# Optimization experiments

Hardware: AMD Instinct MI355X
Metric: run time of the kernel (lower is better)

The kernel has to match this reference:

```python
import jax, jax.numpy as jnp
import numpy as np

KG_E = 50000
KG_R = 500
E_DIM = 300
NE = 400000      # entity-entity adjacency nnz
NEER = 400000    # entity-entity-relation triples
ALPHA1 = 0.1
ALPHA2 = 0.3
LRELU_ALPHA = 0.2


def setup_inputs() -> dict:
    key = jax.random.key(0)
    ks = jax.random.split(key, 13)
    primal_e_0 = jax.random.normal(ks[0], (KG_E, E_DIM), jnp.float32)
    # sparse-ish relation->entity incidence matrices (dense storage as in torch code)
    r_head = (jax.random.uniform(ks[1], (KG_R, KG_E)) < 0.01).astype(jnp.float32)
    r_tail = (jax.random.uniform(ks[2], (KG_R, KG_E)) < 0.01).astype(jnp.float32)
    e_adj_index = jax.random.randint(ks[3], (2, NE), 0, KG_E)
    e_adj_data = jax.random.uniform(ks[4], (NE,), jnp.float32)
    eer_adj_index = jax.random.randint(ks[5], (2, NEER), 0, KG_E)
    eer_adj_data = jax.random.randint(ks[6], (NEER,), 0, KG_R)
    s = 0.05
    be_L = jax.random.normal(ks[7], (KG_E, 1), jnp.float32) * s
    be_R = jax.random.normal(ks[8], (KG_E, 1), jnp.float32) * s
    atten_r = jax.random.normal(ks[9], (2 * E_DIM, 1), jnp.float32) * s
    gcnW1 = jax.random.normal(ks[10], (E_DIM, E_DIM), jnp.float32) * s
    highwayWr = jax.random.normal(ks[11], (E_DIM, E_DIM), jnp.float32) * s
    highwaybr = jax.random.normal(ks[12], (E_DIM, 1), jnp.float32) * s
    return {"primal_e_0": primal_e_0, "r_head": r_head, "r_tail": r_tail,
            "e_adj_data": e_adj_data, "be_L": be_L, "be_R": be_R,
            "atten_r": atten_r, "gcnW1": gcnW1, "highwayWr": highwayWr,
            "highwaybr": highwaybr, "e_adj_index": e_adj_index,
            "eer_adj_index": eer_adj_index, "eer_adj_data": eer_adj_data}


def _spmm(idx, data, x):
    # sparse [KG_E, KG_E] (COO rows=idx[0], cols=idx[1], vals=data) @ dense x
    rows, cols = idx[0], idx[1]
    return jax.ops.segment_sum(data[:, None] * x[cols], rows, num_segments=KG_E)


def _inv_or_zero(x):
    return jnp.where(x == 0, 0.0, 1.0 / x)


def _add_r_layer(e, be_L, be_R, r_head, r_tail, rh_inv, rt_inv):
    L_r = (r_head @ (e * be_L)) * rh_inv   # [KG_R, E_DIM]
    R_r = (r_tail @ (e * be_R)) * rt_inv
    return jax.nn.relu(jnp.concatenate([L_r, R_r], axis=-1))  # [KG_R, 2*E_DIM]


def _add_e_att_layer(e, r_layer, eer_idx, eer_rel, atten_r):
    rows, cols = eer_idx[0], eer_idx[1]
    e_ij = jnp.concatenate([e[rows], e[cols]], axis=1)           # [NEER, 2*E_DIM]
    eer_embed = e_ij * r_layer[eer_rel]                           # [NEER, 2*E_DIM]
    score = (eer_embed @ atten_r)[:, 0]                           # [NEER]
    ee_atten = jnp.exp(-jax.nn.leaky_relu(score, LRELU_ALPHA))
    e_rowsum = jax.ops.segment_sum(ee_atten, rows, num_segments=KG_E)[:, None]
    e_rowsum = _inv_or_zero(e_rowsum)
    e_out = jax.ops.segment_sum(ee_atten[:, None] * e[cols], rows, num_segments=KG_E)
    return jax.nn.relu(e_out * e_rowsum)


def _add_diag_layer(e, gcnW1, e_adj_index, e_adj_data):
    # dropout p=0 (eval) -> identity
    return jax.nn.relu(_spmm(e_adj_index, e_adj_data, e @ gcnW1))


def _highway(e1, e2, Wr, br):
    gate = jax.nn.sigmoid(e1 @ Wr + br[:, 0])
    return gate * e2 + (1.0 - gate) * e1


def reference(primal_e_0, r_head, r_tail, e_adj_data, be_L, be_R, atten_r,
              gcnW1, highwayWr, highwaybr, e_adj_index, eer_adj_index,
              eer_adj_data):
    rh_inv = _inv_or_zero(jnp.sum(r_head, axis=-1, keepdims=True))
    rt_inv = _inv_or_zero(jnp.sum(r_tail, axis=-1, keepdims=True))
    name_embed = primal_e_0
    r1 = _add_r_layer(name_embed, be_L, be_R, r_head, r_tail, rh_inv, rt_inv)
    e1 = _add_e_att_layer(name_embed, r1, eer_adj_index, eer_adj_data, atten_r)
    e1 = name_embed + ALPHA1 * e1
    r2 = _add_r_layer(e1, be_L, be_R, r_head, r_tail, rh_inv, rt_inv)
    e2 = _add_e_att_layer(e1, r2, eer_adj_index, eer_adj_data, atten_r)
    e2 = name_embed + ALPHA2 * e2
    g1 = _add_diag_layer(e2, gcnW1, e_adj_index, e_adj_data)
    g2 = _highway(e2, g1, highwayWr, highwaybr)
    g3 = _add_diag_layer(g2, gcnW1, e_adj_index, e_adj_data)
    return _highway(g2, g3, highwayWr, highwaybr)
```

## Files before the change

### kernel.cpp

```cpp
#include <hip/hip_runtime.h>
#include <hip/hip_fp16.h>
#include <math.h>

#define KG_E  50000
#define KG_R  500
#define E_DIM 300
#define NPAIR 150
#define NP2   75
#define CAP   1024
#define LRELU 0.2f

#define NK    10
#define NT    40
#define XS_LD 328

#define NB_SCAN 49

typedef __attribute__((ext_vector_type(8))) _Float16 f16x8;
typedef __attribute__((ext_vector_type(4))) float f32x4;

__device__ __forceinline__ __half2 u2h2(unsigned u) {
  union { unsigned u; __half2 h; } v; v.u = u; return v.h;
}
__device__ __forceinline__ unsigned h22u(__half2 h) {
  union { unsigned u; __half2 h; } v; v.h = h; return v.u;
}
__device__ __forceinline__ float hlo(unsigned u) { return __low2float(u2h2(u)); }
__device__ __forceinline__ float hhi(unsigned u) { return __high2float(u2h2(u)); }
__device__ __forceinline__ unsigned packh(float lo, float hi) {
  return h22u(__floats2half2_rn(lo, hi));
}

__global__ __launch_bounds__(256) void k_toh(
    const float* __restrict__ src, __half* __restrict__ dst, int n4)
{
  int i = blockIdx.x * 256 + threadIdx.x;
  if (i >= n4) return;
  float4 f = ((const float4*)src)[i];
  uint2 o;
  o.x = packh(f.x, f.y);
  o.y = packh(f.z, f.w);
  ((uint2*)dst)[i] = o;
}

#define NCH 5
#define SCAP 1024
#define NF4 2500
__global__ __launch_bounds__(256) void k_compact2(
    const float* __restrict__ r_head, const float* __restrict__ r_tail,
    const float* __restrict__ be_L, const float* __restrict__ be_R,
    int* __restrict__ lidx, float* __restrict__ lsval,
    int* __restrict__ fill, float* __restrict__ rsum)
{
  __shared__ int   ls_e[SCAP];
  __shared__ float ls_v[SCAP];
  __shared__ int   ls_cnt;
  __shared__ float ls_sum;
  __shared__ int   ls_base;
  int m = blockIdx.z;
  int r = blockIdx.y;
  const float* rowp = (m ? r_tail : r_head) + (size_t)r * KG_E;
  const float* be   = m ? be_R : be_L;
  int slot = m * KG_R + r;
  int lane = threadIdx.x & 63;
  if (threadIdx.x == 0) { ls_cnt = 0; ls_sum = 0.f; }
  __syncthreads();

  const int CH = KG_E / NCH;
  int c0 = blockIdx.x * CH;
  const float4* rp4 = (const float4*)(rowp + c0);
  float lsum = 0.f;

  #pragma unroll
  for (int i = 0; i < (NF4 + 1023) / 1024; ++i) {
    int fi0 = i * 1024 + threadIdx.x;
    float vals[16];
    #pragma unroll
    for (int k = 0; k < 4; ++k) {
      int fi = fi0 + k * 256;
      float4 f = (fi < NF4) ? rp4[fi] : make_float4(0.f, 0.f, 0.f, 0.f);
      vals[k*4+0] = f.x; vals[k*4+1] = f.y; vals[k*4+2] = f.z; vals[k*4+3] = f.w;
    }
    int cnt16 = 0;
    #pragma unroll
    for (int q = 0; q < 16; ++q) {
      lsum += vals[q];
      cnt16 += (vals[q] != 0.f) ? 1 : 0;
    }
    int pre = cnt16;
    #pragma unroll
    for (int off = 1; off < 64; off <<= 1) {
      int u = __shfl_up(pre, off, 64);
      if (lane >= off) pre += u;
    }
    int wave_base = 0;
    if (lane == 63 && pre > 0) wave_base = atomicAdd(&ls_cnt, pre);
    wave_base = __shfl(wave_base, 63, 64);
    if (cnt16 > 0) {
      int o = wave_base + pre - cnt16;
      #pragma unroll
      for (int k = 0; k < 4; ++k) {
        int fi = fi0 + k * 256;
        #pragma unroll
        for (int q = 0; q < 4; ++q) {
          float v = vals[k*4+q];
          if (v != 0.f) {
            if (o < SCAP) {
              int e = c0 + fi * 4 + q;
              ls_e[o] = e;
              ls_v[o] = v * be[e];
            }
            ++o;
          }
        }
      }
    }
  }
  #pragma unroll
  for (int off = 32; off > 0; off >>= 1) lsum += __shfl_xor(lsum, off, 64);
  if (lane == 0 && lsum != 0.f) atomicAdd(&ls_sum, lsum);
  __syncthreads();

  int total = ls_cnt < SCAP ? ls_cnt : SCAP;
  if (threadIdx.x == 0) {
    ls_base = atomicAdd(&fill[slot], total);
    if (ls_sum != 0.f) atomicAdd(&rsum[slot], ls_sum);
  }
  __syncthreads();
  int gbase = ls_base;
  int*   li = lidx  + (size_t)slot * CAP;
  float* lv = lsval + (size_t)slot * CAP;
  for (int i = threadIdx.x; i < total; i += 256) {
    int pos = gbase + i;
    if (pos < CAP) { li[pos] = ls_e[i]; lv[pos] = ls_v[i]; }
  }
}

__global__ __launch_bounds__(256) void k_rmeta(
    const int* __restrict__ fill, const float* __restrict__ rsum,
    int* __restrict__ cnt, float* __restrict__ inv)
{
  int i = blockIdx.x * 256 + threadIdx.x;
  if (i < 2 * KG_R) {
    int c = fill[i];
    cnt[i] = c > CAP ? CAP : c;
    float s = rsum[i];
    inv[i] = (s == 0.f) ? 0.f : 1.f / s;
  }
}

__global__ __launch_bounds__(192) void k_rlayer(
    const __half* __restrict__ Eb, const int* __restrict__ lidx,
    const float* __restrict__ lsval, const int* __restrict__ cnt,
    const float* __restrict__ inv, const float* __restrict__ atten,
    unsigned* __restrict__ wpk)
{
  int b = blockIdx.x;
  int m = b / KG_R, r = b % KG_R;
  int p = threadIdx.x;
  if (p >= NPAIR) return;
  int slot = m * KG_R + r;
  int n = cnt[slot];
  const int*   li = lidx  + (size_t)slot * CAP;
  const float* lv = lsval + (size_t)slot * CAP;
  float alo = 0.f, ahi = 0.f;
  #pragma unroll 4
  for (int i = 0; i < n; ++i) {
    int e = li[i];
    float s = lv[i];
    unsigned u = ((const unsigned*)(Eb + (size_t)e * E_DIM))[p];
    alo += s * hlo(u);
    ahi += s * hhi(u);
  }
  float iv = inv[slot];
  float vlo = alo * iv; vlo = vlo > 0.f ? vlo : 0.f;
  float vhi = ahi * iv; vhi = vhi > 0.f ? vhi : 0.f;
  vlo *= atten[m * E_DIM + 2 * p];
  vhi *= atten[m * E_DIM + 2 * p + 1];
  wpk[(size_t)slot * NPAIR + p] = packh(vlo, vhi);
}

__global__ __launch_bounds__(256) void k_hist(
    const int* __restrict__ rows, int* __restrict__ cnt, int n)
{
  int i = blockIdx.x * 256 + threadIdx.x;
  if (i < n) atomicAdd(&cnt[rows[i]], 1);
}

__global__ __launch_bounds__(256) void k_scan_a(
    const int* __restrict__ c0, const int* __restrict__ c1,
    int* __restrict__ bsum, int n)
{
  const int* c = blockIdx.y ? c1 : c0;
  int base = blockIdx.x * 1024;
  int s = 0;
  #pragma unroll
  for (int k = 0; k < 4; ++k) {
    int i = base + k * 256 + threadIdx.x;
    if (i < n) s += c[i];
  }
  #pragma unroll
  for (int off = 32; off > 0; off >>= 1) s += __shfl_xor(s, off, 64);
  __shared__ int ws[4];
  if ((threadIdx.x & 63) == 0) ws[threadIdx.x >> 6] = s;
  __syncthreads();
  if (threadIdx.x == 0)
    bsum[blockIdx.y * (NB_SCAN + 1) + blockIdx.x] = ws[0] + ws[1] + ws[2] + ws[3];
}

__global__ __launch_bounds__(64) void k_scan_b(int* __restrict__ bsum)
{
  if (threadIdx.x < 2) {
    int* b = bsum + threadIdx.x * (NB_SCAN + 1);
    int acc = 0;
    for (int i = 0; i < NB_SCAN; ++i) { int v = b[i]; b[i] = acc; acc += v; }
    b[NB_SCAN] = acc;
  }
}

__global__ __launch_bounds__(256) void k_scan_c(
    const int* __restrict__ c0, const int* __restrict__ c1,
    const int* __restrict__ bsum,
    int* __restrict__ s0, int* __restrict__ s1, int n)
{
  const int* c = blockIdx.y ? c1 : c0;
  int* sO = blockIdx.y ? s1 : s0;
  if (blockIdx.x == 0 && threadIdx.x == 0)
    sO[n] = bsum[blockIdx.y * (NB_SCAN + 1) + NB_SCAN];
  int boff = bsum[blockIdx.y * (NB_SCAN + 1) + blockIdx.x];
  int i0 = blockIdx.x * 1024 + threadIdx.x * 4;
  int4 v = {0, 0, 0, 0};
  if (i0 < n) v = ((const int4*)c)[i0 >> 2];
  int tsum = v.x + v.y + v.z + v.w;
  int lane = threadIdx.x & 63, wid = threadIdx.x >> 6;
  int inc = tsum;
  #pragma unroll
  for (int off = 1; off < 64; off <<= 1) {
    int u = __shfl_up(inc, off, 64);
    if (lane >= off) inc += u;
  }
  __shared__ int ws[4];
  if (lane == 63) ws[wid] = inc;
  __syncthreads();
  int woff = 0;
  if (wid > 0) woff += ws[0];
  if (wid > 1) woff += ws[1];
  if (wid > 2) woff += ws[2];
  int ex = boff + woff + inc - tsum;
  if (i0 < n) {
    int4 o;
    o.x = ex; o.y = ex + v.x; o.z = o.y + v.y; o.w = o.z + v.z;
    ((int4*)sO)[i0 >> 2] = o;
  }
}

__global__ __launch_bounds__(256) void k_scatter_eer(
    const int* __restrict__ eidx, const int* __restrict__ erel,
    const int* __restrict__ start, int* __restrict__ fill,
    int* __restrict__ scol, int* __restrict__ srel, int neer)
{
  int i = blockIdx.x * 256 + threadIdx.x;
  if (i >= neer) return;
  int row = eidx[i];
  int pos = start[row] + atomicAdd(&fill[row], 1);
  scol[pos] = eidx[neer + i];
  srel[pos] = erel[i];
}

__global__ __launch_bounds__(256) void k_scatter_adj(
    const int* __restrict__ aidx, const float* __restrict__ adata,
    const int* __restrict__ start, int* __restrict__ fill,
    int* __restrict__ scol, float* __restrict__ sval, int ne)
{
  int i = blockIdx.x * 256 + threadIdx.x;
  if (i >= ne) return;
  int row = aidx[i];
  int pos = start[row] + atomicAdd(&fill[row], 1);
  scol[pos] = aidx[ne + i];
  sval[pos] = adata[i];
}

__global__ __launch_bounds__(256) void k_att_csr(
    const __half* __restrict__ Eb, const unsigned* __restrict__ wpk,
    const int* __restrict__ start, const int* __restrict__ scol,
    const int* __restrict__ srel, const __half* __restrict__ baseb,
    float alpha, __half* __restrict__ outb)
{
  int wave = threadIdx.x >> 6, lane = threadIdx.x & 63;
  int half = lane >> 5, hl = lane & 31;
  int row = blockIdx.x * 4 + wave;
  if (row >= KG_E) return;
  int s = start[row], e = start[row + 1];
  const uint2* erp = (const uint2*)(Eb + (size_t)row * E_DIM);
  __half2 zero2 = __floats2half2_rn(0.f, 0.f);
  __half2 er[3][2], ac[3][2];
  #pragma unroll
  for (int c = 0; c < 3; ++c) {
    int m = c * 32 + hl;
    if (m < NP2) {
      uint2 u = erp[m];
      er[c][0] = u2h2(u.x); er[c][1] = u2h2(u.y);
    } else { er[c][0] = zero2; er[c][1] = zero2; }
    ac[c][0] = zero2; ac[c][1] = zero2;
  }
  float rs = 0.f;
  int nIter = (e - s + 1) >> 1;

  bool actA = false; int relA = 0;
  uint2 CA[3];
  #pragma unroll
  for (int c = 0; c < 3; ++c) CA[c] = make_uint2(0u, 0u);
  {
    int j0 = s + half;
    if (nIter > 0 && j0 < e) {
      actA = true;
      int col = scol[j0]; relA = srel[j0];
      const uint2* ecp = (const uint2*)(Eb + (size_t)col * E_DIM);
      #pragma unroll
      for (int c = 0; c < 3; ++c) {
        int m = c * 32 + hl;
        if (m < NP2) CA[c] = ecp[m];
      }
    }
  }

  for (int it = 0; it < nIter; ++it) {
    bool actB = false; int relB = 0;
    uint2 CB[3];
    #pragma unroll
    for (int c = 0; c < 3; ++c) CB[c] = make_uint2(0u, 0u);
    {
      int jn = s + 2 * (it + 1) + half;
      if (it + 1 < nIter && jn < e) {
        actB = true;
        int col = scol[jn]; relB = srel[jn];
        const uint2* ecp = (const uint2*)(Eb + (size_t)col * E_DIM);
        #pragma unroll
        for (int c = 0; c < 3; ++c) {
          int m = c * 32 + hl;
          if (m < NP2) CB[c] = ecp[m];
        }
      }
    }
    const uint2* whp = (const uint2*)(wpk + (size_t)relA * NPAIR);
    const uint2* wtp = (const uint2*)(wpk + (size_t)(KG_R + relA) * NPAIR);
    __half2 p2a = zero2, p2b = zero2;
    #pragma unroll
    for (int c = 0; c < 3; ++c) {
      int m = c * 32 + hl;
      if (m < NP2) {
        uint2 uh = whp[m], ut = wtp[m];
        p2a = __hfma2(er[c][0], u2h2(uh.x), p2a);
        p2b = __hfma2(er[c][1], u2h2(uh.y), p2b);
        p2a = __hfma2(u2h2(CA[c].x), u2h2(ut.x), p2a);
        p2b = __hfma2(u2h2(CA[c].y), u2h2(ut.y), p2b);
      }
    }
    __half2 p2 = __hadd2(p2a, p2b);
    float p4 = __low2float(p2) + __high2float(p2);
    #pragma unroll
    for (int off = 16; off > 0; off >>= 1) p4 += __shfl_xor(p4, off, 64);
    float la = p4 >= 0.f ? p4 : LRELU * p4;
    float at = actA ? __expf(-la) : 0.f;
    rs += at;
    __half2 at2 = __float2half2_rn(at);
    #pragma unroll
    for (int c = 0; c < 3; ++c) {
      ac[c][0] = __hfma2(at2, u2h2(CA[c].x), ac[c][0]);
      ac[c][1] = __hfma2(at2, u2h2(CA[c].y), ac[c][1]);
    }
    actA = actB; relA = relB;
    #pragma unroll
    for (int c = 0; c < 3; ++c) CA[c] = CB[c];
  }
  rs += __shfl_xor(rs, 32, 64);
  #pragma unroll
  for (int c = 0; c < 3; ++c) {
    #pragma unroll
    for (int k = 0; k < 2; ++k) {
      unsigned o = __shfl_xor(h22u(ac[c][k]), 32, 64);
      ac[c][k] = __hadd2(ac[c][k], u2h2(o));
    }
  }
  if (half == 0) {
    float iv = (rs == 0.f) ? 0.f : 1.f / rs;
    const uint2* bp = (const uint2*)(baseb + (size_t)row * E_DIM);
    uint2* op = (uint2*)(outb + (size_t)row * E_DIM);
    #pragma unroll
    for (int c = 0; c < 3; ++c) {
      int m = c * 32 + hl;
      if (m < NP2) {
        uint2 ub = bp[m];
        float v0 = __low2float(ac[c][0]) * iv;  v0 = v0 > 0.f ? v0 : 0.f;
        float v1 = __high2float(ac[c][0]) * iv; v1 = v1 > 0.f ? v1 : 0.f;
        float v2 = __low2float(ac[c][1]) * iv;  v2 = v2 > 0.f ? v2 : 0.f;
        float v3 = __high2float(ac[c][1]) * iv; v3 = v3 > 0.f ? v3 : 0.f;
        uint2 o2;
        o2.x = packh(hlo(ub.x) + alpha * v0, hhi(ub.x) + alpha * v1);
        o2.y = packh(hlo(ub.y) + alpha * v2, hhi(ub.y) + alpha * v3);
        op[m] = o2;
      }
    }
  }
}

__global__ __launch_bounds__(256) void k_spmm_hw(
    const __half* __restrict__ Xb, const int* __restrict__ start,
    const int* __restrict__ scol, const float* __restrict__ sval,
    const __half* __restrict__ Gb, const __half* __restrict__ baseb,
    const float* __restrict__ br,
    __half* __restrict__ outb, float* __restrict__ outf)
{
  int wave = threadIdx.x >> 6, lane = threadIdx.x & 63;
  int half = lane >> 5, hl = lane & 31;
  int row = blockIdx.x * 4 + wave;
  if (row >= KG_E) return;
  int s = start[row], e = start[row + 1];
  float ac0[3] = {0,0,0}, ac1[3] = {0,0,0}, ac2[3] = {0,0,0}, ac3[3] = {0,0,0};
  int nIter = (e - s + 1) >> 1;

  float vA = 0.f;
  uint2 XA[3];
  #pragma unroll
  for (int c = 0; c < 3; ++c) XA[c] = make_uint2(0u, 0u);
  {
    int j0 = s + half;
    if (nIter > 0 && j0 < e) {
      int col = scol[j0]; vA = sval[j0];
      const uint2* xp = (const uint2*)(Xb + (size_t)col * E_DIM);
      #pragma unroll
      for (int c = 0; c < 3; ++c) {
        int m = c * 32 + hl;
        if (m < NP2) XA[c] = xp[m];
      }
    }
  }
  for (int it = 0; it < nIter; ++it) {
    float vB = 0.f;
    uint2 XB[3];
    #pragma unroll
    for (int c = 0; c < 3; ++c) XB[c] = make_uint2(0u, 0u);
    {
      int jn = s + 2 * (it + 1) + half;
      if (it + 1 < nIter && jn < e) {
        int col = scol[jn]; vB = sval[jn];
        const uint2* xp = (const uint2*)(Xb + (size_t)col * E_DIM);
        #pragma unroll
        for (int c = 0; c < 3; ++c) {
          int m = c * 32 + hl;
          if (m < NP2) XB[c] = xp[m];
        }
      }
    }
    #pragma unroll
    for (int c = 0; c < 3; ++c) {
      ac0[c] += vA * hlo(XA[c].x); ac1[c] += vA * hhi(XA[c].x);
      ac2[c] += vA * hlo(XA[c].y); ac3[c] += vA * hhi(XA[c].y);
    }
    vA = vB;
    #pragma unroll
    for (int c = 0; c < 3; ++c) XA[c] = XB[c];
  }
  #pragma unroll
  for (int c = 0; c < 3; ++c) {
    ac0[c] += __shfl_xor(ac0[c], 32, 64);
    ac1[c] += __shfl_xor(ac1[c], 32, 64);
    ac2[c] += __shfl_xor(ac2[c], 32, 64);
    ac3[c] += __shfl_xor(ac3[c], 32, 64);
  }
  if (half == 0) {
    const uint2* gp = (const uint2*)(Gb + (size_t)row * E_DIM);
    const uint2* bp = (const uint2*)(baseb + (size_t)row * E_DIM);
    #pragma unroll
    for (int c = 0; c < 3; ++c) {
      int m = c * 32 + hl;
      if (m < NP2) {
        uint2 ug = gp[m], ub = bp[m];
        float4 b4 = ((const float4*)br)[m];
        float g0 = 1.f / (1.f + __expf(-(hlo(ug.x) + b4.x)));
        float g1 = 1.f / (1.f + __expf(-(hhi(ug.x) + b4.y)));
        float g2 = 1.f / (1.f + __expf(-(hlo(ug.y) + b4.z)));
        float g3 = 1.f / (1.f + __expf(-(hhi(ug.y) + b4.w)));
        float y0 = ac0[c] > 0.f ? ac0[c] : 0.f;
        float y1 = ac1[c] > 0.f ? ac1[c] : 0.f;
        float y2 = ac2[c] > 0.f ? ac2[c] : 0.f;
        float y3 = ac3[c] > 0.f ? ac3[c] : 0.f;
        float o0 = g0 * y0 + (1.f - g0) * hlo(ub.x);
        float o1 = g1 * y1 + (1.f - g1) * hhi(ub.x);
        float o2 = g2 * y2 + (1.f - g2) * hlo(ub.y);
        float o3 = g3 * y3 + (1.f - g3) * hhi(ub.y);
        if (outb) {
          uint2 ov;
          ov.x = packh(o0, o1); ov.y = packh(o2, o3);
          ((uint2*)(outb + (size_t)row * E_DIM))[m] = ov;
        } else {
          float4 of; of.x = o0; of.y = o1; of.z = o2; of.w = o3;
          ((float4*)(outf + (size_t)row * E_DIM))[m] = of;
        }
      }
    }
  }
}

__global__ __launch_bounds__(64) void k_packW(
    const float* __restrict__ W1, const float* __restrict__ W2,
    __half* __restrict__ Wp)
{
  int lane = threadIdx.x;
  int t = blockIdx.x, s = blockIdx.y;
  int c = t * 16 + (lane & 15);
  __half v[8];
  #pragma unroll
  for (int j = 0; j < 8; ++j) {
    int k = s * 32 + (lane >> 4) * 8 + j;
    float x = 0.f;
    if (k < E_DIM && c < 2 * E_DIM)
      x = (c < E_DIM) ? W1[(size_t)k * E_DIM + c]
                      : W2[(size_t)k * E_DIM + (c - E_DIM)];
    v[j] = __float2half_rn(x);
  }
  size_t base = ((size_t)(t * NK + s) * 64 + lane) * 8;
  #pragma unroll
  for (int j = 0; j < 8; ++j) Wp[base + j] = v[j];
}

__global__ __launch_bounds__(256) void k_gemm2_mfma(
    const __half* __restrict__ Xb, const __half* __restrict__ Wp,
    __half* __restrict__ Y1, __half* __restrict__ Y2, int M)
{
  __shared__ __half Xs[32][XS_LD];
  int tid = threadIdx.x;
  int r0 = blockIdx.x * 32;
  int nb = blockIdx.y;

  for (int t = tid; t < 32 * (XS_LD / 2); t += 256) {
    int r = t / (XS_LD / 2), u = t % (XS_LD / 2);
    unsigned v = 0;
    int rg = r0 + r;
    if (rg < M && u < E_DIM / 2) v = ((const unsigned*)Xb)[(size_t)rg * (E_DIM / 2) + u];
    ((unsigned*)&Xs[0][0])[r * (XS_LD / 2) + u] = v;
  }
  __syncthreads();

  int wid = tid >> 6, lane = tid & 63;
  int wave_m = wid >> 1, wave_n = wid & 1;
  int rowA = wave_m * 16 + (lane & 15);
  int kgrp = (lane >> 4) * 8;
  int tb0 = nb * 8 + wave_n * 4;

  const f16x8* wfrag = (const f16x8*)Wp + (size_t)tb0 * (NK * 64) + lane;

  f32x4 acc[4] = {{0,0,0,0},{0,0,0,0},{0,0,0,0},{0,0,0,0}};
  #pragma unroll 2
  for (int ks = 0; ks < NK; ++ks) {
    f16x8 a = *(const f16x8*)&Xs[rowA][ks * 32 + kgrp];
    #pragma unroll
    for (int nt = 0; nt < 4; ++nt) {
      f16x8 b = wfrag[(nt * NK + ks) * 64];
      acc[nt] = __builtin_amdgcn_mfma_f32_16x16x32_f16(a, b, acc[nt], 0, 0, 0);
    }
  }

  int rbase = r0 + wave_m * 16 + ((lane >> 4) << 2);
  #pragma unroll
  for (int nt = 0; nt < 4; ++nt) {
    int c = (tb0 + nt) * 16 + (lane & 15);
    #pragma unroll
    for (int j = 0; j < 4; ++j) {
      int row = rbase + j;
      if (row < M) {
        __half hv = __float2half_rn(acc[nt][j]);
        if (c < E_DIM)            Y1[(size_t)row * E_DIM + c] = hv;
        else if (c < 2 * E_DIM)   Y2[(size_t)row * E_DIM + (c - E_DIM)] = hv;
      }
    }
  }
}

extern "C" void kernel_launch(void* const* d_in, const int* in_sizes, int n_in,
                              void* d_out, int out_size, void* d_ws, size_t ws_size,
                              hipStream_t stream)
{
  const float* primal      = (const float*)d_in[0];
  const float* r_head      = (const float*)d_in[1];
  const float* r_tail      = (const float*)d_in[2];
  const float* e_adj_data  = (const float*)d_in[3];
  const float* be_L        = (const float*)d_in[4];
  const float* be_R        = (const float*)d_in[5];
  const float* atten_r     = (const float*)d_in[6];
  const float* gcnW1       = (const float*)d_in[7];
  const float* hwWr        = (const float*)d_in[8];
  const float* hwbr        = (const float*)d_in[9];
  const int*   e_adj_index = (const int*)d_in[10];
  const int*   eer_idx     = (const int*)d_in[11];
  const int*   eer_rel     = (const int*)d_in[12];
  int ne   = in_sizes[10] / 2;
  int neer = in_sizes[11] / 2;

  char* ws = (char*)d_ws;
  size_t off = 0;
  auto take = [&](size_t bytes) {
    void* p = ws + off;
    off = (off + bytes + 255) & ~(size_t)255;
    return p;
  };
  int*   cnt      = (int*)  take((size_t)2 * KG_R * sizeof(int));
  float* inv      = (float*)take((size_t)2 * KG_R * sizeof(float));
  size_t z0 = off;
  int*   hcntA    = (int*)  take((size_t)KG_E * sizeof(int));
  int*   hcntB    = (int*)  take((size_t)KG_E * sizeof(int));
  int*   hfillA   = (int*)  take((size_t)KG_E * sizeof(int));
  int*   hfillB   = (int*)  take((size_t)KG_E * sizeof(int));
  int*   rfill    = (int*)  take((size_t)2 * KG_R * sizeof(int));
  float* rsumb    = (float*)take((size_t)2 * KG_R * sizeof(float));
  size_t z1 = off;
  int*   lidx     = (int*)  take((size_t)2 * KG_R * CAP * sizeof(int));
  float* lsv      = (float*)take((size_t)2 * KG_R * CAP * sizeof(float));
  unsigned* wpk   = (unsigned*)take((size_t)2 * KG_R * NPAIR * sizeof(unsigned));
  int*   bsum     = (int*)  take((size_t)2 * (NB_SCAN + 1) * sizeof(int));
  int*   eer_start= (int*)  take((size_t)(KG_E + 4) * sizeof(int));
  int*   adj_start= (int*)  take((size_t)(KG_E + 4) * sizeof(int));
  int*   eer_scol = (int*)  take((size_t)neer * sizeof(int));
  int*   eer_srel = (int*)  take((size_t)neer * sizeof(int));
  int*   adj_scol = (int*)  take((size_t)ne * sizeof(int));
  float* adj_sval = (float*)take((size_t)ne * sizeof(float));
  __half* Wp = (__half*)take((size_t)NT * NK * 64 * 8 * sizeof(__half));
  __half* B0 = (__half*)take((size_t)KG_E * E_DIM * sizeof(__half));
  __half* B1 = (__half*)take((size_t)KG_E * E_DIM * sizeof(__half));
  __half* B2 = (__half*)take((size_t)KG_E * E_DIM * sizeof(__half));
  __half* Fb = (__half*)take((size_t)KG_E * E_DIM * sizeof(__half));
  __half* Gb = (__half*)take((size_t)KG_E * E_DIM * sizeof(__half));
  float* out      = (float*)d_out;
  (void)ws_size; (void)n_in; (void)out_size;

  int eg = (neer + 255) / 256;
  int ag = (ne + 255) / 256;

  hipMemsetAsync(ws + z0, 0, z1 - z0, stream);

  k_hist<<<eg, 256, 0, stream>>>(eer_idx, hcntA, neer);
  k_hist<<<ag, 256, 0, stream>>>(e_adj_index, hcntB, ne);
  k_scan_a<<<dim3(NB_SCAN, 2), 256, 0, stream>>>(hcntA, hcntB, bsum, KG_E);
  k_scan_b<<<1, 64, 0, stream>>>(bsum);
  k_scan_c<<<dim3(NB_SCAN, 2), 256, 0, stream>>>(hcntA, hcntB, bsum,
                                                 eer_start, adj_start, KG_E);
  k_scatter_eer<<<eg, 256, 0, stream>>>(eer_idx, eer_rel, eer_start, hfillA,
                                        eer_scol, eer_srel, neer);
  k_scatter_adj<<<ag, 256, 0, stream>>>(e_adj_index, e_adj_data, adj_start, hfillB,
                                        adj_scol, adj_sval, ne);

  k_compact2<<<dim3(NCH, KG_R, 2), 256, 0, stream>>>(r_head, r_tail, be_L, be_R,
                                                     lidx, lsv, rfill, rsumb);
  k_rmeta<<<(2 * KG_R + 255) / 256, 256, 0, stream>>>(rfill, rsumb, cnt, inv);
  k_packW<<<dim3(NT, NK), 64, 0, stream>>>(gcnW1, hwWr, Wp);
  int n4 = KG_E * E_DIM / 4;
  k_toh<<<(n4 + 255) / 256, 256, 0, stream>>>(primal, B0, n4);

  int rg = (KG_E + 3) / 4;

  k_rlayer<<<2 * KG_R, 192, 0, stream>>>(B0, lidx, lsv, cnt, inv, atten_r, wpk);
  k_att_csr<<<rg, 256, 0, stream>>>(B0, wpk, eer_start, eer_scol, eer_srel,
                                    B0, 0.1f, B1);
  k_rlayer<<<2 * KG_R, 192, 0, stream>>>(B1, lidx, lsv, cnt, inv, atten_r, wpk);
  k_att_csr<<<rg, 256, 0, stream>>>(B1, wpk, eer_start, eer_scol, eer_srel,
                                    B0, 0.3f, B2);

  dim3 gg((KG_E + 31) / 32, 5);
  k_gemm2_mfma<<<gg, 256, 0, stream>>>(B2, Wp, Fb, Gb, KG_E);
  k_spmm_hw<<<rg, 256, 0, stream>>>(Fb, adj_start, adj_scol, adj_sval,
                                    Gb, B2, hwbr, B1, (float*)nullptr);

  k_gemm2_mfma<<<gg, 256, 0, stream>>>(B1, Wp, Fb, Gb, KG_E);
  k_spmm_hw<<<rg, 256, 0, stream>>>(Fb, adj_start, adj_scol, adj_sval,
                                    Gb, B1, hwbr, (__half*)nullptr, out);
}
```

Before: 766.7 us.

## Reuse staged X tile across all GEMM column blocks and batch compaction loads

The dual GEMM kernel now loads each 32-row X tile into shared memory once and loops over all five column blocks inside the block, with the A fragments held in registers. Before, a separate grid dimension re-staged the same tile for every column block. The compaction kernel now issues all twelve float4 loads per thread up front and does a single wave prefix-scan and atomic, replacing one per chunk of four loads. In exchange, register pressure is higher and there are five times fewer GEMM blocks, which may reduce occupancy or parallelism.

Result: slower. 828.3 us (+8.0%).

```diff
diff --git a/kernel.cpp b/kernel.cpp
--- a/kernel.cpp
+++ b/kernel.cpp
@@ -69,49 +69,45 @@
   const int CH = KG_E / NCH;
   int c0 = blockIdx.x * CH;
   const float4* rp4 = (const float4*)(rowp + c0);
+
+  float vals[48];
+  #pragma unroll
+  for (int t = 0; t < 12; ++t) {
+    int fi = t * 256 + threadIdx.x;
+    float4 f = (fi < NF4) ? rp4[fi] : make_float4(0.f, 0.f, 0.f, 0.f);
+    vals[t*4+0] = f.x; vals[t*4+1] = f.y; vals[t*4+2] = f.z; vals[t*4+3] = f.w;
+  }
   float lsum = 0.f;
-
-  #pragma unroll
-  for (int i = 0; i < (NF4 + 1023) / 1024; ++i) {
-    int fi0 = i * 1024 + threadIdx.x;
-    float vals[16];
-    #pragma unroll
-    for (int k = 0; k < 4; ++k) {
-      int fi = fi0 + k * 256;
-      float4 f = (fi < NF4) ? rp4[fi] : make_float4(0.f, 0.f, 0.f, 0.f);
-      vals[k*4+0] = f.x; vals[k*4+1] = f.y; vals[k*4+2] = f.z; vals[k*4+3] = f.w;
-    }
-    int cnt16 = 0;
-    #pragma unroll
-    for (int q = 0; q < 16; ++q) {
-      lsum += vals[q];
-      cnt16 += (vals[q] != 0.f) ? 1 : 0;
-    }
-    int pre = cnt16;
-    #pragma unroll
-    for (int off = 1; off < 64; off <<= 1) {
-      int u = __shfl_up(pre, off, 64);
-      if (lane >= off) pre += u;
-    }
-    int wave_base = 0;
-    if (lane == 63 && pre > 0) wave_base = atomicAdd(&ls_cnt, pre);
-    wave_base = __shfl(wave_base, 63, 64);
-    if (cnt16 > 0) {
-      int o = wave_base + pre - cnt16;
+  int cnt = 0;
+  #pragma unroll
+  for (int q = 0; q < 48; ++q) {
+    lsum += vals[q];
+    cnt += (vals[q] != 0.f) ? 1 : 0;
+  }
+  int pre = cnt;
+  #pragma unroll
+  for (int off = 1; off < 64; off <<= 1) {
+    int u = __shfl_up(pre, off, 64);
+    if (lane >= off) pre += u;
+  }
+  int wave_base = 0;
+  if (lane == 63 && pre > 0) wave_base = atomicAdd(&ls_cnt, pre);
+  wave_base = __shfl(wave_base, 63, 64);
+  if (cnt > 0) {
+    int o = wave_base + pre - cnt;
+    #pragma unroll
+    for (int t = 0; t < 12; ++t) {
+      int fi = t * 256 + threadIdx.x;
       #pragma unroll
-      for (int k = 0; k < 4; ++k) {
-        int fi = fi0 + k * 256;
-        #pragma unroll
-        for (int q = 0; q < 4; ++q) {
-          float v = vals[k*4+q];
-          if (v != 0.f) {
-            if (o < SCAP) {
-              int e = c0 + fi * 4 + q;
-              ls_e[o] = e;
-              ls_v[o] = v * be[e];
-            }
-            ++o;
+      for (int q = 0; q < 4; ++q) {
+        float v = vals[t*4+q];
+        if (v != 0.f) {
+          if (o < SCAP) {
+            int e = c0 + fi * 4 + q;
+            ls_e[o] = e;
+            ls_v[o] = v * be[e];
           }
+          ++o;
         }
       }
     }
@@ -531,7 +527,6 @@
   __shared__ __half Xs[32][XS_LD];
   int tid = threadIdx.x;
   int r0 = blockIdx.x * 32;
-  int nb = blockIdx.y;
 
   for (int t = tid; t < 32 * (XS_LD / 2); t += 256) {
     int r = t / (XS_LD / 2), u = t % (XS_LD / 2);
@@ -546,32 +541,36 @@
   int wave_m = wid >> 1, wave_n = wid & 1;
   int rowA = wave_m * 16 + (lane & 15);
   int kgrp = (lane >> 4) * 8;
-  int tb0 = nb * 8 + wave_n * 4;
-
-  const f16x8* wfrag = (const f16x8*)Wp + (size_t)tb0 * (NK * 64) + lane;
-
-  f32x4 acc[4] = {{0,0,0,0},{0,0,0,0},{0,0,0,0},{0,0,0,0}};
-  #pragma unroll 2
-  for (int ks = 0; ks < NK; ++ks) {
-    f16x8 a = *(const f16x8*)&Xs[rowA][ks * 32 + kgrp];
+  int rbase = r0 + wave_m * 16 + ((lane >> 4) << 2);
+
+  f16x8 afrag[NK];
+  #pragma unroll
+  for (int ks = 0; ks < NK; ++ks)
+    afrag[ks] = *(const f16x8*)&Xs[rowA][ks * 32 + kgrp];
+
+  for (int nb = 0; nb < 5; ++nb) {
+    int tb0 = nb * 8 + wave_n * 4;
+    const f16x8* wfrag = (const f16x8*)Wp + (size_t)tb0 * (NK * 64) + lane;
+    f32x4 acc[4] = {{0,0,0,0},{0,0,0,0},{0,0,0,0},{0,0,0,0}};
+    #pragma unroll 2
+    for (int ks = 0; ks < NK; ++ks) {
+      #pragma unroll
+      for (int nt = 0; nt < 4; ++nt) {
+        f16x8 b = wfrag[(nt * NK + ks) * 64];
+        acc[nt] = __builtin_amdgcn_mfma_f32_16x16x32_f16(afrag[ks], b, acc[nt], 0, 0, 0);
+      }
+    }
     #pragma unroll
     for (int nt = 0; nt < 4; ++nt) {
-      f16x8 b = wfrag[(nt * NK + ks) * 64];
-      acc[nt] = __builtin_amdgcn_mfma_f32_16x16x32_f16(a, b, acc[nt], 0, 0, 0);
-    }
-  }
-
-  int rbase = r0 + wave_m * 16 + ((lane >> 4) << 2);
-  #pragma unroll
-  for (int nt = 0; nt < 4; ++nt) {
-    int c = (tb0 + nt) * 16 + (lane & 15);
-    #pragma unroll
-    for (int j = 0; j < 4; ++j) {
-      int row = rbase + j;
-      if (row < M) {
-        __half hv = __float2half_rn(acc[nt][j]);
-        if (c < E_DIM)            Y1[(size_t)row * E_DIM + c] = hv;
-        else if (c < 2 * E_DIM)   Y2[(size_t)row * E_DIM + (c - E_DIM)] = hv;
+      int c = (tb0 + nt) * 16 + (lane & 15);
+      #pragma unroll
+      for (int j = 0; j < 4; ++j) {
+        int row = rbase + j;
+        if (row < M) {
+          __half hv = __float2half_rn(acc[nt][j]);
+          if (c < E_DIM)            Y1[(size_t)row * E_DIM + c] = hv;
+          else if (c < 2 * E_DIM)   Y2[(size_t)row * E_DIM + (c - E_DIM)] = hv;
+        }
       }
     }
   }
@@ -665,12 +664,12 @@
   k_att_csr<<<rg, 256, 0, stream>>>(B1, wpk, eer_start, eer_scol, eer_srel,
                                     B0, 0.3f, B2);
 
-  dim3 gg((KG_E + 31) / 32, 5);
-  k_gemm2_mfma<<<gg, 256, 0, stream>>>(B2, Wp, Fb, Gb, KG_E);
+  int gemm_grid = (KG_E + 31) / 32;
+  k_gemm2_mfma<<<gemm_grid, 256, 0, stream>>>(B2, Wp, Fb, Gb, KG_E);
   k_spmm_hw<<<rg, 256, 0, stream>>>(Fb, adj_start, adj_scol, adj_sval,
                                     Gb, B2, hwbr, B1, (float*)nullptr);
 
-  k_gemm2_mfma<<<gg, 256, 0, stream>>>(B1, Wp, Fb, Gb, KG_E);
+  k_gemm2_mfma<<<gemm_grid, 256, 0, stream>>>(B1, Wp, Fb, Gb, KG_E);
   k_spmm_hw<<<rg, 256, 0, stream>>>(Fb, adj_start, adj_scol, adj_sval,
                                     Gb, B1, hwbr, (__half*)nullptr, out);
 }
```
